# Optimization experiments

Measured on AMD Instinct MI355X. Metric: run time of the kernel, lower is better.

The kernel has to match this reference:

```python
import jax, jax.numpy as jnp
import numpy as np
from jax import lax

B, H, W = 4096, 8, 8
DICT, SE, E, NZ = 64, 8, 256, 1024
C1, C2 = 64, 128
EPS = 1e-4


def setup_inputs() -> dict:
    key = jax.random.key(0)
    ks = jax.random.split(key, 32)
    d = {}
    d['s'] = jax.random.randint(ks[0], (B, H, W), 0, DICT)
    d['s_prime'] = jax.random.randint(ks[1], (B, H, W), 0, DICT)
    d['w_embed'] = jax.random.normal(ks[2], (DICT, SE), dtype=jnp.float32)
    i = 3
    for p in ('p1', 'p2', 'p3'):
        d[p + '_w1'] = jax.random.normal(ks[i], (C1, SE, 3, 3), dtype=jnp.float32) * 0.1; i += 1
        d[p + '_b1'] = jax.random.normal(ks[i], (C1,), dtype=jnp.float32) * 0.1; i += 1
        d[p + '_w2'] = jax.random.normal(ks[i], (C2, C1, 3, 3), dtype=jnp.float32) * 0.05; i += 1
        d[p + '_b2'] = jax.random.normal(ks[i], (C2,), dtype=jnp.float32) * 0.05; i += 1
        d[p + '_lw'] = jax.random.normal(ks[i], (E, C2 * H * W), dtype=jnp.float32) * 0.02; i += 1
        d[p + '_lb'] = jax.random.normal(ks[i], (E,), dtype=jnp.float32) * 0.02; i += 1
    d['z_vectors'] = jax.random.normal(ks[i], (NZ, E), dtype=jnp.float32)
    d['scale'] = jnp.ones((1,), dtype=jnp.float32)
    return d


def _conv(x, w, b):
    # x: [B,C,H,W], w: [O,I,3,3], padding=1 == SAME for k=3
    y = lax.conv_general_dilated(x, w, (1, 1), 'SAME',
                                 dimension_numbers=('NCHW', 'OIHW', 'NCHW'))
    return y + b[None, :, None, None]


def _phi(x, w1, b1, w2, b2, lw, lb):
    # run_modules(..., last_activation=True): relu after every conv
    x = jax.nn.relu(_conv(x, w1, b1))
    x = jax.nn.relu(_conv(x, w2, b2))
    x = x.reshape(x.shape[0], -1)  # [B, C2*H*W]
    return x @ lw.T + lb  # [B, E]


def _normalized(m, eps):
    return m / (jnp.sqrt(jnp.sum(m * m, axis=1, keepdims=True)) + eps)


def reference(s, s_prime, w_embed,
              p1_w1, p1_b1, p1_w2, p1_b2, p1_lw, p1_lb,
              p2_w1, p2_b1, p2_w2, p2_b2, p2_lw, p2_lb,
              p3_w1, p3_b1, p3_w2, p3_b2, p3_lw, p3_lb,
              z_vectors, scale):
    # nn.Embedding(max_norm=1): renorm rows with norm > 1 to unit norm
    wn = jnp.sqrt(jnp.sum(w_embed * w_embed, axis=1, keepdims=True))
    w = w_embed * jnp.minimum(1.0, 1.0 / jnp.maximum(wn, 1e-7))
    s_embed = jnp.transpose(w[s], (0, 3, 1, 2))        # [B,SE,H,W]
    sp_embed = jnp.transpose(w[s_prime], (0, 3, 1, 2))  # embed_conv is None -> identity

    s_int = _phi(s_embed, p1_w1, p1_b1, p1_w2, p1_b2, p1_lw, p1_lb)            # phi1
    diff_int = _phi(sp_embed - s_embed, p2_w1, p2_b1, p2_w2, p2_b2, p2_lw, p2_lb)  # phi2
    sp_out = _normalized(_phi(sp_embed, p3_w1, p3_b1, p3_w2, p3_b2, p3_lw, p3_lb), EPS)  # phi3

    # quantize: cdist (p=2) against codebook, argmax (farthest, as in source), gather
    x2 = jnp.sum(diff_int * diff_int, axis=1, keepdims=True)      # [B,1]
    z2 = jnp.sum(z_vectors * z_vectors, axis=1)[None, :]          # [1,NZ]
    dist = jnp.sqrt(jnp.maximum(x2 + z2 - 2.0 * (diff_int @ z_vectors.T), 0.0))  # [B,NZ]
    z_inds = jnp.argmax(dist, axis=1)                              # [B]
    z_matrix = z_vectors[z_inds]                                   # [B,E]

    s_out = _normalized(s_int + z_matrix, EPS)                     # fc (fc_sizes=None)
    gram = s_out @ sp_out.T                                        # [B,B]
    return jnp.exp(scale) * gram
```

## Files before the change

### kernel.cpp

```cpp
#include <hip/hip_runtime.h>
#include <hip/hip_bf16.h>
#include <math.h>

#define NB 4096
#define SE 8
#define ND 64
#define C1 64
#define C2 128
#define NE 256
#define NZ 1024
#define CHUNK 2048
#define KACT 8192
#define KSPLIT 8

#define W1M_N (3*64*96)
#define W2M_N (3*128*576)
#define ZT_N  (256*1024)
#define PREP_TOTAL (W1M_N + W2M_N + ZT_N)
#define LW_N (NE*KACT)

typedef __attribute__((ext_vector_type(8))) short bf16x8;
typedef __attribute__((ext_vector_type(4))) float f32x4;
typedef __attribute__((ext_vector_type(8))) unsigned short u16x8;
typedef __attribute__((ext_vector_type(4))) unsigned short u16x4;

static __device__ __forceinline__ unsigned short f2bf(float v) {
  __hip_bfloat16 h = __float2bfloat16(v);
  return __builtin_bit_cast(unsigned short, h);
}
static __device__ __forceinline__ float bf2f(unsigned short u) {
  return __bfloat162float(__builtin_bit_cast(__hip_bfloat16, u));
}

__global__ __launch_bounds__(256) void prep_kernel(
    const float* __restrict__ w1_0, const float* __restrict__ w1_1, const float* __restrict__ w1_2,
    const float* __restrict__ w2_0, const float* __restrict__ w2_1, const float* __restrict__ w2_2,
    const float* __restrict__ z,
    unsigned short* __restrict__ w1mh, unsigned short* __restrict__ w1ml,
    unsigned short* __restrict__ w2mh, unsigned short* __restrict__ w2ml,
    float* __restrict__ zT)
{
  int idx = blockIdx.x * 256 + threadIdx.x;
  if (idx < W1M_N) {
    int p = idx / 6144; int r = idx - p*6144; int o = r / 96; int q = r - o*96;
    int j = q >> 3; int c = q & 7;
    const float* w1 = (p == 0) ? w1_0 : (p == 1) ? w1_1 : w1_2;
    float v = (j < 9) ? w1[o*72 + c*9 + j] : 0.f;
    unsigned short h = f2bf(v);
    w1mh[idx] = h;
    w1ml[idx] = f2bf(v - bf2f(h));
  } else if (idx < W1M_N + W2M_N) {
    int r0 = idx - W1M_N;
    int p = r0 / (128*576); int r = r0 - p*(128*576);
    int o = r / 576; int rem = r - o*576; int j = rem >> 6; int c = rem & 63;
    const float* w2 = (p == 0) ? w2_0 : (p == 1) ? w2_1 : w2_2;
    float v = w2[o*576 + c*9 + j];
    unsigned short h = f2bf(v);
    w2mh[r0] = h;
    w2ml[r0] = f2bf(v - bf2f(h));
  } else if (idx < PREP_TOTAL) {
    int r = idx - (W1M_N + W2M_N);
    int e = r >> 10, n = r & 1023;
    zT[r] = z[n*256 + e];
  }
}

__global__ __launch_bounds__(256) void prep_lw_kernel(
    const float* __restrict__ lw, unsigned short* __restrict__ lwh,
    unsigned short* __restrict__ lwl, int do_lo)
{
  int idx = blockIdx.x * 256 + threadIdx.x;
  float v = lw[idx];
  unsigned short h = f2bf(v);
  lwh[idx] = h;
  if (do_lo) lwl[idx] = f2bf(v - bf2f(h));
}

template<int PASSES>
__global__ __launch_bounds__(256, 2) void conv_phi_kernel(
    const int* __restrict__ s, const int* __restrict__ sp,
    const float* __restrict__ w_embed,
    const unsigned short* __restrict__ w1mh, const unsigned short* __restrict__ w1ml,
    const float* __restrict__ b1,
    const unsigned short* __restrict__ w2mh, const unsigned short* __restrict__ w2ml,
    const float* __restrict__ b2,
    unsigned short* __restrict__ acth, unsigned short* __restrict__ actl,
    int mode, int b_start)
{
  __shared__ float wtab[ND][SE];
  __shared__ int sidx[128];
  __shared__ int spidx[128];
  __shared__ __align__(16) unsigned short xph[2][960];
  __shared__ __align__(16) unsigned short xpl[2][960];
  __shared__ __align__(16) unsigned short c1h[2][7680];
  __shared__ __align__(16) unsigned short c1l[2][7680];

  const int tid = threadIdx.x;
  const int b0 = b_start + blockIdx.x * 2;

  {
    int4 z4 = {0,0,0,0};
    for (int t = tid; t < 240; t += 256) { ((int4*)xph)[t] = z4; ((int4*)xpl)[t] = z4; }
    for (int t = tid; t < 1920; t += 256) { ((int4*)c1h)[t] = z4; ((int4*)c1l)[t] = z4; }
  }

  if (tid < 128) sidx[tid] = s[b0*64 + tid];
  else spidx[tid - 128] = sp[b0*64 + tid - 128];
  if (tid < 64) {
    float v[SE]; float ss = 0.f;
    #pragma unroll
    for (int c = 0; c < SE; ++c) { v[c] = w_embed[tid*SE + c]; ss += v[c]*v[c]; }
    float nrm = sqrtf(ss);
    float sc = fminf(1.f, 1.f / fmaxf(nrm, 1e-7f));
    #pragma unroll
    for (int c = 0; c < SE; ++c) wtab[tid][c] = v[c] * sc;
  }
  __syncthreads();

  if (tid < 128) {
    const int im = tid >> 6;
    const int p = tid & 63;
    const int y = p >> 3, x = p & 7;
    const float* r0 = wtab[sidx[tid]];
    const float* r1 = wtab[spidx[tid]];
    u16x8 hv, lv;
    #pragma unroll
    for (int c = 0; c < SE; ++c) {
      float e0 = r0[c], e1 = r1[c];
      float v = (mode == 0) ? e0 : (mode == 1) ? (e1 - e0) : e1;
      unsigned short h = f2bf(v);
      hv[c] = h;
      lv[c] = f2bf(v - bf2f(h));
    }
    const int lin = (y + 1)*12 + (x + 1);
    *(u16x8*)(&xph[im][lin*8]) = hv;
    *(u16x8*)(&xpl[im][lin*8]) = lv;
  }
  __syncthreads();

  {
    const int lane = tid & 63, wid = tid >> 6;
    const int im = wid >> 1, ph = wid & 1;
    const int l15 = lane & 15, lk4 = lane >> 4;

    f32x4 a1[4][2];
    #pragma unroll
    for (int fm = 0; fm < 4; ++fm)
      #pragma unroll
      for (int nf = 0; nf < 2; ++nf) a1[fm][nf] = (f32x4){0.f,0.f,0.f,0.f};

    #pragma unroll
    for (int kk = 0; kk < 3; ++kk) {
      const int j = (kk << 2) + lk4;
      const int jc = (j > 8) ? 8 : j;
      const int dy = jc / 3, dx = jc - 3*(jc/3);
      bf16x8 Wh[4], Wl[4];
      #pragma unroll
      for (int fm = 0; fm < 4; ++fm) {
        const int o = (fm << 4) + l15;
        Wh[fm] = *(const bf16x8*)(w1mh + o*96 + (kk << 5) + (lk4 << 3));
        Wl[fm] = *(const bf16x8*)(w1ml + o*96 + (kk << 5) + (lk4 << 3));
      }
      #pragma unroll
      for (int nf = 0; nf < 2; ++nf) {
        const int p = (ph << 5) + (nf << 4) + l15;
        const int lin = ((p >> 3) + dy)*12 + (p & 7) + dx;
        const bf16x8 Xh = *(const bf16x8*)(&xph[im][lin << 3]);
        const bf16x8 Xl = *(const bf16x8*)(&xpl[im][lin << 3]);
        __builtin_amdgcn_s_setprio(1);
        #pragma unroll
        for (int fm = 0; fm < 4; ++fm) {
          a1[fm][nf] = __builtin_amdgcn_mfma_f32_16x16x32_bf16(Wh[fm], Xh, a1[fm][nf], 0, 0, 0);
          a1[fm][nf] = __builtin_amdgcn_mfma_f32_16x16x32_bf16(Wl[fm], Xh, a1[fm][nf], 0, 0, 0);
          a1[fm][nf] = __builtin_amdgcn_mfma_f32_16x16x32_bf16(Wh[fm], Xl, a1[fm][nf], 0, 0, 0);
        }
        __builtin_amdgcn_s_setprio(0);
      }
    }

    #pragma unroll
    for (int fm = 0; fm < 4; ++fm) {
      const int obase = (fm << 4) + (lk4 << 2);
      const float4 bv = *(const float4*)(b1 + obase);
      const int cb = obase >> 3;
      const int osub = obase & 7;
      #pragma unroll
      for (int nf = 0; nf < 2; ++nf) {
        const int p = (ph << 5) + (nf << 4) + l15;
        const int lin = ((p >> 3) + 1)*12 + (p & 7) + 1;
        const int idx2 = (lin << 6) + ((cb ^ (lin & 7)) << 3) + osub;
        u16x4 hv, lv;
        {
          float v0 = fmaxf(a1[fm][nf][0] + bv.x, 0.f);
          float v1 = fmaxf(a1[fm][nf][1] + bv.y, 0.f);
          float v2 = fmaxf(a1[fm][nf][2] + bv.z, 0.f);
          float v3 = fmaxf(a1[fm][nf][3] + bv.w, 0.f);
          hv[0] = f2bf(v0); hv[1] = f2bf(v1); hv[2] = f2bf(v2); hv[3] = f2bf(v3);
          lv[0] = f2bf(v0 - bf2f(hv[0])); lv[1] = f2bf(v1 - bf2f(hv[1]));
          lv[2] = f2bf(v2 - bf2f(hv[2])); lv[3] = f2bf(v3 - bf2f(hv[3]));
        }
        *(u16x4*)(&c1h[im][idx2]) = hv;
        *(u16x4*)(&c1l[im][idx2]) = lv;
      }
    }
  }
  __syncthreads();

  {
    const int lane = tid & 63, wid = tid >> 6;
    const int im = wid >> 1;
    const int ob = (wid & 1) << 6;
    const int l15 = lane & 15, lk4 = lane >> 4;
    const int y0b = l15 >> 3, x0 = l15 & 7;

    f32x4 acc[4][4];
    #pragma unroll
    for (int mf = 0; mf < 4; ++mf)
      #pragma unroll
      for (int nf = 0; nf < 4; ++nf) acc[mf][nf] = (f32x4){0.f,0.f,0.f,0.f};

    #pragma unroll
    for (int j = 0; j < 9; ++j) {
      const int dy = j / 3, dx = j - 3*(j/3);
      #pragma unroll
      for (int h2 = 0; h2 < 2; ++h2) {
        const int kofs = j*64 + h2*32 + lk4*8;
        bf16x8 Bh[4], Bl[4];
        #pragma unroll
        for (int nf = 0; nf < 4; ++nf) {
          const int orow = ob + (nf << 4) + l15;
          Bh[nf] = *(const bf16x8*)(w2mh + orow*576 + kofs);
          if (PASSES == 3) Bl[nf] = *(const bf16x8*)(w2ml + orow*576 + kofs);
        }
        const int cbk = (h2 << 2) + lk4;
        bf16x8 Ah[4], Al[4];
        #pragma unroll
        for (int mf = 0; mf < 4; ++mf) {
          const int lin = ((mf << 1) + y0b + dy)*12 + x0 + dx;
          const int idx2 = (lin << 6) + ((cbk ^ (lin & 7)) << 3);
          Ah[mf] = *(const bf16x8*)(&c1h[im][idx2]);
          Al[mf] = *(const bf16x8*)(&c1l[im][idx2]);
        }
        __builtin_amdgcn_s_setprio(1);
        #pragma unroll
        for (int mf = 0; mf < 4; ++mf) {
          #pragma unroll
          for (int nf = 0; nf < 4; ++nf) {
            acc[mf][nf] = __builtin_amdgcn_mfma_f32_16x16x32_bf16(Ah[mf], Bh[nf], acc[mf][nf], 0, 0, 0);
            acc[mf][nf] = __builtin_amdgcn_mfma_f32_16x16x32_bf16(Al[mf], Bh[nf], acc[mf][nf], 0, 0, 0);
            if (PASSES == 3)
              acc[mf][nf] = __builtin_amdgcn_mfma_f32_16x16x32_bf16(Ah[mf], Bl[nf], acc[mf][nf], 0, 0, 0);
          }
        }
        __builtin_amdgcn_s_setprio(0);
      }
    }

    const size_t rowbase = (size_t)(blockIdx.x*2 + im) * 8192;
    #pragma unroll
    for (int nf = 0; nf < 4; ++nf) {
      const int col = ob + (nf << 4) + l15;
      const float bv = b2[col];
      #pragma unroll
      for (int mf = 0; mf < 4; ++mf) {
        const int p0 = mf*16 + lk4*4;
        u16x4 hv, lv;
        #pragma unroll
        for (int r2 = 0; r2 < 4; ++r2) {
          float v = fmaxf(acc[mf][nf][r2] + bv, 0.f);
          unsigned short hq = f2bf(v);
          hv[r2] = hq;
          lv[r2] = f2bf(v - bf2f(hq));
        }
        *(u16x4*)(acth + rowbase + col*64 + p0) = hv;
        if (PASSES == 3)
          *(u16x4*)(actl + rowbase + col*64 + p0) = lv;
      }
    }
  }
}

template<int PASSES>
__global__ __launch_bounds__(256) void gemm_lds_tn(
    const unsigned short* __restrict__ Ahp, const unsigned short* __restrict__ Alp,
    const unsigned short* __restrict__ Bhp, const unsigned short* __restrict__ Blp,
    int K, float* __restrict__ Cdirect, float* __restrict__ Cpart,
    const float* __restrict__ bias, const float* __restrict__ scale_ptr)
{
  constexpr int NOP = (PASSES == 3) ? 2 : 1;
  __shared__ __align__(16) unsigned short As[NOP][128*64];
  __shared__ __align__(16) unsigned short Bs[NOP][64*64];

  const int tid = threadIdx.x;
  const int lane = tid & 63, wid = tid >> 6;
  const int wm = wid >> 1, wn = wid & 1;
  const int l15 = lane & 15, lk4 = lane >> 4;
  const int M = gridDim.x << 7, N = gridDim.y << 6;
  const int KC = K / gridDim.z;
  const int bm = blockIdx.x << 7, bn = blockIdx.y << 6;
  const int kbase = blockIdx.z * KC;
  const int NT = KC >> 6;

  const int sr = tid >> 3;
  const int sc8 = (tid & 7) * 8;

  const unsigned short* gA[NOP];
  const unsigned short* gB[NOP];
  gA[0] = Ahp; gB[0] = Bhp;
  if (PASSES == 3) { gA[1] = Alp; gB[1] = Blp; }

  u16x8 ra[NOP][4], rb[NOP][2];

  f32x4 acc[4][2];
  #pragma unroll
  for (int fm = 0; fm < 4; ++fm)
    #pragma unroll
    for (int nf = 0; nf < 2; ++nf) acc[fm][nf] = (f32x4){0.f,0.f,0.f,0.f};

  {
    const int k0 = kbase + sc8;
    #pragma unroll
    for (int p = 0; p < NOP; ++p) {
      #pragma unroll
      for (int i = 0; i < 4; ++i)
        ra[p][i] = *(const u16x8*)(gA[p] + (size_t)(bm + sr + i*32) * K + k0);
      #pragma unroll
      for (int i = 0; i < 2; ++i)
        rb[p][i] = *(const u16x8*)(gB[p] + (size_t)(bn + sr + i*32) * K + k0);
    }
  }

  for (int t = 0; t < NT; ++t) {
    __syncthreads();
    #pragma unroll
    for (int p = 0; p < NOP; ++p) {
      #pragma unroll
      for (int i = 0; i < 4; ++i) {
        const int r = sr + i*32;
        *(u16x8*)(&As[p][r*64 + (sc8 ^ ((r & 7) << 3))]) = ra[p][i];
      }
      #pragma unroll
      for (int i = 0; i < 2; ++i) {
        const int r = sr + i*32;
        *(u16x8*)(&Bs[p][r*64 + (sc8 ^ ((r & 7) << 3))]) = rb[p][i];
      }
    }
    __syncthreads();
    if (t + 1 < NT) {
      const int k0 = kbase + ((t + 1) << 6) + sc8;
      #pragma unroll
      for (int p = 0; p < NOP; ++p) {
        #pragma unroll
        for (int i = 0; i < 4; ++i)
          ra[p][i] = *(const u16x8*)(gA[p] + (size_t)(bm + sr + i*32) * K + k0);
        #pragma unroll
        for (int i = 0; i < 2; ++i)
          rb[p][i] = *(const u16x8*)(gB[p] + (size_t)(bn + sr + i*32) * K + k0);
      }
    }
    #pragma unroll
    for (int ks = 0; ks < 2; ++ks) {
      const int kb = ks*32 + lk4*8;
      bf16x8 af[NOP][4], bf[NOP][2];
      #pragma unroll
      for (int p = 0; p < NOP; ++p) {
        #pragma unroll
        for (int fm = 0; fm < 4; ++fm) {
          const int r = wm*64 + fm*16 + l15;
          af[p][fm] = *(const bf16x8*)(&As[p][r*64 + (kb ^ ((r & 7) << 3))]);
        }
        #pragma unroll
        for (int nf = 0; nf < 2; ++nf) {
          const int r = wn*32 + nf*16 + l15;
          bf[p][nf] = *(const bf16x8*)(&Bs[p][r*64 + (kb ^ ((r & 7) << 3))]);
        }
      }
      #pragma unroll
      for (int fm = 0; fm < 4; ++fm) {
        #pragma unroll
        for (int nf = 0; nf < 2; ++nf) {
          acc[fm][nf] = __builtin_amdgcn_mfma_f32_16x16x32_bf16(af[0][fm], bf[0][nf], acc[fm][nf], 0, 0, 0);
          if (PASSES == 3) {
            acc[fm][nf] = __builtin_amdgcn_mfma_f32_16x16x32_bf16(af[0][fm], bf[1][nf], acc[fm][nf], 0, 0, 0);
            acc[fm][nf] = __builtin_amdgcn_mfma_f32_16x16x32_bf16(af[1][fm], bf[0][nf], acc[fm][nf], 0, 0, 0);
          }
        }
      }
    }
  }

  if (Cpart) {
    float* base = Cpart + (size_t)blockIdx.z * ((size_t)M * N);
    #pragma unroll
    for (int fm = 0; fm < 4; ++fm) {
      #pragma unroll
      for (int nf = 0; nf < 2; ++nf) {
        const int row0 = bm + wm*64 + fm*16 + lk4*4;
        const int col  = bn + wn*32 + nf*16 + l15;
        #pragma unroll
        for (int r2 = 0; r2 < 4; ++r2)
          base[(size_t)(row0 + r2) * N + col] = acc[fm][nf][r2];
      }
    }
  } else {
    float alpha = scale_ptr ? expf(scale_ptr[0]) : 1.f;
    #pragma unroll
    for (int fm = 0; fm < 4; ++fm) {
      #pragma unroll
      for (int nf = 0; nf < 2; ++nf) {
        const int row0 = bm + wm*64 + fm*16 + lk4*4;
        const int col  = bn + wn*32 + nf*16 + l15;
        const float bv = bias ? bias[col] : 0.f;
        #pragma unroll
        for (int r2 = 0; r2 < 4; ++r2)
          Cdirect[(size_t)(row0 + r2) * N + col] = alpha * acc[fm][nf][r2] + bv;
      }
    }
  }
}

__global__ __launch_bounds__(256) void reduce_bias_kernel(
    const float* __restrict__ part, const float* __restrict__ bias, float* __restrict__ out)
{
  const int idx = blockIdx.x * 256 + threadIdx.x;
  float a = bias[idx & (NE-1)];
  #pragma unroll
  for (int q = 0; q < KSPLIT; ++q) a += part[(size_t)q * (CHUNK*NE) + idx];
  out[idx] = a;
}

__global__ __launch_bounds__(256) void quant_kernel(
    const float* __restrict__ diff, const float* __restrict__ zT, int* __restrict__ z_ind)
{
  __shared__ __align__(16) float d[8][NE];
  __shared__ float wv[8][4];
  __shared__ int wni[8][4];
  const int tid = threadIdx.x;
  const int b0 = blockIdx.x * 8;
  for (int j = tid; j < 8*NE; j += 256) (&d[0][0])[j] = diff[(size_t)b0*NE + j];
  __syncthreads();

  float zz[4] = {0.f, 0.f, 0.f, 0.f};
  float dot[8][4] = {};
  for (int e = 0; e < NE; e += 4) {
    float4 dd[8];
    #pragma unroll
    for (int r = 0; r < 8; ++r) dd[r] = *(const float4*)(&d[r][e]);
    #pragma unroll
    for (int u = 0; u < 4; ++u) {
      const float* zr = zT + (size_t)(e + u) * NZ + tid;
      float z0 = zr[0], z1 = zr[256], z2 = zr[512], z3 = zr[768];
      zz[0] = fmaf(z0, z0, zz[0]); zz[1] = fmaf(z1, z1, zz[1]);
      zz[2] = fmaf(z2, z2, zz[2]); zz[3] = fmaf(z3, z3, zz[3]);
      #pragma unroll
      for (int r = 0; r < 8; ++r) {
        const float de = (u == 0) ? dd[r].x : (u == 1) ? dd[r].y : (u == 2) ? dd[r].z : dd[r].w;
        dot[r][0] = fmaf(z0, de, dot[r][0]);
        dot[r][1] = fmaf(z1, de, dot[r][1]);
        dot[r][2] = fmaf(z2, de, dot[r][2]);
        dot[r][3] = fmaf(z3, de, dot[r][3]);
      }
    }
  }

  const int lane = tid & 63, wid = tid >> 6;
  #pragma unroll
  for (int r = 0; r < 8; ++r) {
    float best = zz[0] - 2.f*dot[r][0]; int bi = tid;
    float v1 = zz[1] - 2.f*dot[r][1]; if (v1 > best) { best = v1; bi = tid + 256; }
    float v2 = zz[2] - 2.f*dot[r][2]; if (v2 > best) { best = v2; bi = tid + 512; }
    float v3 = zz[3] - 2.f*dot[r][3]; if (v3 > best) { best = v3; bi = tid + 768; }
    for (int m = 1; m < 64; m <<= 1) {
      float ov = __shfl_xor(best, m, 64);
      int   oi = __shfl_xor(bi, m, 64);
      if (ov > best || (ov == best && oi < bi)) { best = ov; bi = oi; }
    }
    if (lane == 0) { wv[r][wid] = best; wni[r][wid] = bi; }
  }
  __syncthreads();
  if (tid < 8) {
    float best = wv[tid][0]; int bi = wni[tid][0];
    #pragma unroll
    for (int w = 1; w < 4; ++w) {
      float v = wv[tid][w]; int n = wni[tid][w];
      if (v > best || (v == best && n < bi)) { best = v; bi = n; }
    }
    z_ind[b0 + tid] = bi;
  }
}

__global__ __launch_bounds__(256) void norm_to_bf16_kernel(
    const float* __restrict__ v, unsigned short* __restrict__ ob)
{
  const int row = blockIdx.x*4 + (threadIdx.x >> 6);
  const int lane = threadIdx.x & 63;
  float4 x = ((const float4*)v)[(size_t)row*64 + lane];
  float ss = x.x*x.x + x.y*x.y + x.z*x.z + x.w*x.w;
  #pragma unroll
  for (int m = 1; m < 64; m <<= 1) ss += __shfl_xor(ss, m, 64);
  float sc = 1.f / (sqrtf(ss) + 1e-4f);
  u16x4 o;
  o[0] = f2bf(x.x*sc); o[1] = f2bf(x.y*sc); o[2] = f2bf(x.z*sc); o[3] = f2bf(x.w*sc);
  *(u16x4*)(ob + (size_t)row*NE + lane*4) = o;
}

__global__ __launch_bounds__(256) void build_sout_kernel(
    const float* __restrict__ s_int, const float* __restrict__ z,
    const int* __restrict__ z_ind, unsigned short* __restrict__ ob)
{
  const int row = blockIdx.x*4 + (threadIdx.x >> 6);
  const int lane = threadIdx.x & 63;
  const int zi = z_ind[row];
  float4 a = *((const float4*)s_int + (size_t)row*64 + lane);
  float4 c = *((const float4*)z + (size_t)zi*64 + lane);
  float4 x = {a.x + c.x, a.y + c.y, a.z + c.z, a.w + c.w};
  float ss = x.x*x.x + x.y*x.y + x.z*x.z + x.w*x.w;
  #pragma unroll
  for (int m = 1; m < 64; m <<= 1) ss += __shfl_xor(ss, m, 64);
  float sc = 1.f / (sqrtf(ss) + 1e-4f);
  u16x4 o;
  o[0] = f2bf(x.x*sc); o[1] = f2bf(x.y*sc); o[2] = f2bf(x.z*sc); o[3] = f2bf(x.w*sc);
  *(u16x4*)(ob + (size_t)row*NE + lane*4) = o;
}

extern "C" void kernel_launch(void* const* d_in, const int* in_sizes, int n_in,
                              void* d_out, int out_size, void* d_ws, size_t ws_size,
                              hipStream_t stream)
{
  const int* s  = (const int*)d_in[0];
  const int* sp = (const int*)d_in[1];
  const float* w_embed = (const float*)d_in[2];
  const float* z = (const float*)d_in[21];
  const float* scale = (const float*)d_in[22];
  float* out = (float*)d_out;

  size_t off = 0;
  auto allocB = [&](size_t bytes) -> void* {
    void* p = (void*)((char*)d_ws + off);
    off += ((bytes + 255) & ~(size_t)255);
    return p;
  };
  unsigned short* w1mh  = (unsigned short*)allocB((size_t)W1M_N * 2);
  unsigned short* w1ml  = (unsigned short*)allocB((size_t)W1M_N * 2);
  unsigned short* w2mh  = (unsigned short*)allocB((size_t)W2M_N * 2);
  unsigned short* w2ml  = (unsigned short*)allocB((size_t)W2M_N * 2);
  float* zT             = (float*)allocB(ZT_N * 4);
  unsigned short* lwh   = (unsigned short*)allocB((size_t)LW_N * 2);
  unsigned short* lwl   = (unsigned short*)allocB((size_t)LW_N * 2);
  float* s_int          = (float*)allocB((size_t)NB * NE * 4);
  float* diff_int       = (float*)allocB((size_t)NB * NE * 4);
  float* sp_out         = (float*)allocB((size_t)NB * NE * 4);
  unsigned short* soutb = (unsigned short*)allocB((size_t)NB * NE * 2);
  unsigned short* spoutb= (unsigned short*)allocB((size_t)NB * NE * 2);
  int*   z_ind          = (int*)allocB(NB * 4);
  float* part           = (float*)allocB((size_t)CHUNK * NE * KSPLIT * 4);

  unsigned short* acth = (unsigned short*)d_out;
  unsigned short* actl = acth + (size_t)CHUNK * KACT;

  prep_kernel<<<PREP_TOTAL/256, 256, 0, stream>>>(
      (const float*)d_in[3],  (const float*)d_in[9],  (const float*)d_in[15],
      (const float*)d_in[5],  (const float*)d_in[11], (const float*)d_in[17],
      z, w1mh, w1ml, w2mh, w2ml, zT);

  for (int phi = 0; phi < 3; ++phi) {
    const float* b1 = (const float*)d_in[4 + phi*6];
    const float* b2 = (const float*)d_in[6 + phi*6];
    const float* lw = (const float*)d_in[7 + phi*6];
    const float* lb = (const float*)d_in[8 + phi*6];
    float* outvec = (phi == 0) ? s_int : (phi == 1) ? diff_int : sp_out;

    prep_lw_kernel<<<LW_N/256, 256, 0, stream>>>(lw, lwh, lwl, phi == 1);

    for (int b0 = 0; b0 < NB; b0 += CHUNK) {
      if (phi == 1)
        conv_phi_kernel<3><<<CHUNK/2, 256, 0, stream>>>(
            s, sp, w_embed, w1mh + phi*6144, w1ml + phi*6144, b1,
            w2mh + phi*(128*576), w2ml + phi*(128*576), b2,
            acth, actl, phi, b0);
      else
        conv_phi_kernel<2><<<CHUNK/2, 256, 0, stream>>>(
            s, sp, w_embed, w1mh + phi*6144, w1ml + phi*6144, b1,
            w2mh + phi*(128*576), w2ml + phi*(128*576), b2,
            acth, actl, phi, b0);
      dim3 g(CHUNK/128, NE/64, KSPLIT);
      if (phi == 1)
        gemm_lds_tn<3><<<g, 256, 0, stream>>>(acth, actl, lwh, lwl,
            KACT, nullptr, part, nullptr, nullptr);
      else
        gemm_lds_tn<1><<<g, 256, 0, stream>>>(acth, nullptr, lwh, nullptr,
            KACT, nullptr, part, nullptr, nullptr);
      reduce_bias_kernel<<<(CHUNK*NE)/256, 256, 0, stream>>>(part, lb, outvec + (size_t)b0*NE);
    }
  }

  norm_to_bf16_kernel<<<NB/4, 256, 0, stream>>>(sp_out, spoutb);
  quant_kernel<<<NB/8, 256, 0, stream>>>(diff_int, zT, z_ind);
  build_sout_kernel<<<NB/4, 256, 0, stream>>>(s_int, z, z_ind, soutb);

  dim3 gg(NB/128, NB/64, 1);
  gemm_lds_tn<1><<<gg, 256, 0, stream>>>(soutb, nullptr, spoutb, nullptr,
      NE, out, nullptr, nullptr, scale);
}
```

Baseline: 641.8 us.

## Split fused conv kernel into separate conv1 and conv2 kernels via global scratch

The fused conv1+conv2 kernel is split into two kernels. convA computes conv1 for four images per block and writes the bf16 hi/lo activations to a global scratch buffer. convB reads those activations straight from global memory with bounds-checked padding and stages the conv2 weights through swizzled LDS, one 3x3 tap at a time. The aim is lower LDS use and higher occupancy, at the cost of an extra kernel launch and a global round trip for the conv1 activations.

```diff
diff --git a/kernel.cpp b/kernel.cpp
--- a/kernel.cpp
+++ b/kernel.cpp
@@ -76,36 +76,29 @@
   if (do_lo) lwl[idx] = f2bf(v - bf2f(h));
 }
 
-template<int PASSES>
-__global__ __launch_bounds__(256, 2) void conv_phi_kernel(
+__global__ __launch_bounds__(256, 3) void convA_kernel(
     const int* __restrict__ s, const int* __restrict__ sp,
     const float* __restrict__ w_embed,
     const unsigned short* __restrict__ w1mh, const unsigned short* __restrict__ w1ml,
     const float* __restrict__ b1,
-    const unsigned short* __restrict__ w2mh, const unsigned short* __restrict__ w2ml,
-    const float* __restrict__ b2,
-    unsigned short* __restrict__ acth, unsigned short* __restrict__ actl,
+    unsigned short* __restrict__ c1h, unsigned short* __restrict__ c1l,
     int mode, int b_start)
 {
   __shared__ float wtab[ND][SE];
-  __shared__ int sidx[128];
-  __shared__ int spidx[128];
-  __shared__ __align__(16) unsigned short xph[2][960];
-  __shared__ __align__(16) unsigned short xpl[2][960];
-  __shared__ __align__(16) unsigned short c1h[2][7680];
-  __shared__ __align__(16) unsigned short c1l[2][7680];
+  __shared__ __align__(16) unsigned short xph[4][960];
+  __shared__ __align__(16) unsigned short xpl[4][960];
 
   const int tid = threadIdx.x;
-  const int b0 = b_start + blockIdx.x * 2;
+  const int im = tid >> 6, p = tid & 63;
+  const int b = b_start + blockIdx.x*4 + im;
+
+  const int si  = s[b*64 + p];
+  const int spi = sp[b*64 + p];
 
   {
     int4 z4 = {0,0,0,0};
-    for (int t = tid; t < 240; t += 256) { ((int4*)xph)[t] = z4; ((int4*)xpl)[t] = z4; }
-    for (int t = tid; t < 1920; t += 256) { ((int4*)c1h)[t] = z4; ((int4*)c1l)[t] = z4; }
-  }
-
-  if (tid < 128) sidx[tid] = s[b0*64 + tid];
-  else spidx[tid - 128] = sp[b0*64 + tid - 128];
+    for (int t = tid; t < 480; t += 256) { ((int4*)xph)[t] = z4; ((int4*)xpl)[t] = z4; }
+  }
   if (tid < 64) {
     float v[SE]; float ss = 0.f;
     #pragma unroll
@@ -117,12 +110,9 @@
   }
   __syncthreads();
 
-  if (tid < 128) {
-    const int im = tid >> 6;
-    const int p = tid & 63;
-    const int y = p >> 3, x = p & 7;
-    const float* r0 = wtab[sidx[tid]];
-    const float* r1 = wtab[spidx[tid]];
+  {
+    const float* r0 = wtab[si];
+    const float* r1 = wtab[spi];
     u16x8 hv, lv;
     #pragma unroll
     for (int c = 0; c < SE; ++c) {
@@ -132,150 +122,181 @@
       hv[c] = h;
       lv[c] = f2bf(v - bf2f(h));
     }
-    const int lin = (y + 1)*12 + (x + 1);
+    const int lin = ((p >> 3) + 1)*12 + (p & 7) + 1;
     *(u16x8*)(&xph[im][lin*8]) = hv;
     *(u16x8*)(&xpl[im][lin*8]) = lv;
   }
   __syncthreads();
 
-  {
-    const int lane = tid & 63, wid = tid >> 6;
-    const int im = wid >> 1, ph = wid & 1;
-    const int l15 = lane & 15, lk4 = lane >> 4;
-
-    f32x4 a1[4][2];
-    #pragma unroll
-    for (int fm = 0; fm < 4; ++fm)
-      #pragma unroll
-      for (int nf = 0; nf < 2; ++nf) a1[fm][nf] = (f32x4){0.f,0.f,0.f,0.f};
-
-    #pragma unroll
-    for (int kk = 0; kk < 3; ++kk) {
-      const int j = (kk << 2) + lk4;
-      const int jc = (j > 8) ? 8 : j;
-      const int dy = jc / 3, dx = jc - 3*(jc/3);
-      bf16x8 Wh[4], Wl[4];
-      #pragma unroll
-      for (int fm = 0; fm < 4; ++fm) {
-        const int o = (fm << 4) + l15;
-        Wh[fm] = *(const bf16x8*)(w1mh + o*96 + (kk << 5) + (lk4 << 3));
-        Wl[fm] = *(const bf16x8*)(w1ml + o*96 + (kk << 5) + (lk4 << 3));
-      }
-      #pragma unroll
-      for (int nf = 0; nf < 2; ++nf) {
-        const int p = (ph << 5) + (nf << 4) + l15;
-        const int lin = ((p >> 3) + dy)*12 + (p & 7) + dx;
-        const bf16x8 Xh = *(const bf16x8*)(&xph[im][lin << 3]);
-        const bf16x8 Xl = *(const bf16x8*)(&xpl[im][lin << 3]);
-        __builtin_amdgcn_s_setprio(1);
-        #pragma unroll
-        for (int fm = 0; fm < 4; ++fm) {
-          a1[fm][nf] = __builtin_amdgcn_mfma_f32_16x16x32_bf16(Wh[fm], Xh, a1[fm][nf], 0, 0, 0);
-          a1[fm][nf] = __builtin_amdgcn_mfma_f32_16x16x32_bf16(Wl[fm], Xh, a1[fm][nf], 0, 0, 0);
-          a1[fm][nf] = __builtin_amdgcn_mfma_f32_16x16x32_bf16(Wh[fm], Xl, a1[fm][nf], 0, 0, 0);
+  const int lane = tid & 63, wid = tid >> 6;
+  const int l15 = lane & 15, lk4 = lane >> 4;
+
+  f32x4 a1[4][4];
+  #pragma unroll
+  for (int mf = 0; mf < 4; ++mf)
+    #pragma unroll
+    for (int nf = 0; nf < 4; ++nf) a1[mf][nf] = (f32x4){0.f,0.f,0.f,0.f};
+
+  #pragma unroll
+  for (int kk = 0; kk < 3; ++kk) {
+    const int j = (kk << 2) + lk4;
+    const int jc = (j > 8) ? 8 : j;
+    const int dy = jc / 3, dx = jc - 3*(jc/3);
+    bf16x8 Wh[4], Wl[4];
+    #pragma unroll
+    for (int mf = 0; mf < 4; ++mf) {
+      const int o = (mf << 4) + l15;
+      Wh[mf] = *(const bf16x8*)(w1mh + o*96 + (kk << 5) + (lk4 << 3));
+      Wl[mf] = *(const bf16x8*)(w1ml + o*96 + (kk << 5) + (lk4 << 3));
+    }
+    #pragma unroll
+    for (int nf = 0; nf < 4; ++nf) {
+      const int px = (nf << 4) + l15;
+      const int lin = ((px >> 3) + dy)*12 + (px & 7) + dx;
+      const bf16x8 Xh = *(const bf16x8*)(&xph[wid][lin << 3]);
+      const bf16x8 Xl = *(const bf16x8*)(&xpl[wid][lin << 3]);
+      __builtin_amdgcn_s_setprio(1);
+      #pragma unroll
+      for (int mf = 0; mf < 4; ++mf) {
+        a1[mf][nf] = __builtin_amdgcn_mfma_f32_16x16x32_bf16(Wh[mf], Xh, a1[mf][nf], 0, 0, 0);
+        a1[mf][nf] = __builtin_amdgcn_mfma_f32_16x16x32_bf16(Wl[mf], Xh, a1[mf][nf], 0, 0, 0);
+        a1[mf][nf] = __builtin_amdgcn_mfma_f32_16x16x32_bf16(Wh[mf], Xl, a1[mf][nf], 0, 0, 0);
+      }
+      __builtin_amdgcn_s_setprio(0);
+    }
+  }
+
+  const size_t cb = (size_t)(blockIdx.x*4 + wid) * 4096;
+  #pragma unroll
+  for (int mf = 0; mf < 4; ++mf) {
+    const int obase = (mf << 4) + (lk4 << 2);
+    const float4 bv = *(const float4*)(b1 + obase);
+    #pragma unroll
+    for (int nf = 0; nf < 4; ++nf) {
+      const int px = (nf << 4) + l15;
+      u16x4 hv, lv;
+      {
+        float v0 = fmaxf(a1[mf][nf][0] + bv.x, 0.f);
+        float v1 = fmaxf(a1[mf][nf][1] + bv.y, 0.f);
+        float v2 = fmaxf(a1[mf][nf][2] + bv.z, 0.f);
+        float v3 = fmaxf(a1[mf][nf][3] + bv.w, 0.f);
+        hv[0] = f2bf(v0); hv[1] = f2bf(v1); hv[2] = f2bf(v2); hv[3] = f2bf(v3);
+        lv[0] = f2bf(v0 - bf2f(hv[0])); lv[1] = f2bf(v1 - bf2f(hv[1]));
+        lv[2] = f2bf(v2 - bf2f(hv[2])); lv[3] = f2bf(v3 - bf2f(hv[3]));
+      }
+      *(u16x4*)(c1h + cb + px*64 + obase) = hv;
+      *(u16x4*)(c1l + cb + px*64 + obase) = lv;
+    }
+  }
+}
+
+template<int PASSES>
+__global__ __launch_bounds__(256, PASSES==3?2:3) void convB_kernel(
+    const unsigned short* __restrict__ c1h, const unsigned short* __restrict__ c1l,
+    const unsigned short* __restrict__ w2mh, const unsigned short* __restrict__ w2ml,
+    const float* __restrict__ b2,
+    unsigned short* __restrict__ acth, unsigned short* __restrict__ actl)
+{
+  __shared__ __align__(16) unsigned short Bsh[8192];
+  __shared__ __align__(16) unsigned short Bsl[PASSES==3 ? 8192 : 16];
+
+  const int tid = threadIdx.x;
+  const int lane = tid & 63, wid = tid >> 6;
+  const int img = blockIdx.x*2 + (wid >> 1);
+  const int ob = (wid & 1) << 6;
+  const int l15 = lane & 15, lk4 = lane >> 4;
+  const unsigned short* __restrict__ ch = c1h + (size_t)img*4096;
+  const unsigned short* __restrict__ cl = c1l + (size_t)img*4096;
+
+  const int so = tid >> 1;
+  const int sq = (tid & 1) << 5;
+
+  auto stage = [&](int j) {
+    const unsigned short* bh = w2mh + so*576 + j*64;
+    const unsigned short* bl = w2ml + so*576 + j*64;
+    #pragma unroll
+    for (int q = 0; q < 4; ++q) {
+      const int c = sq + q*8;
+      const int d = so*64 + (c ^ ((so & 7) << 3));
+      *(u16x8*)(&Bsh[d]) = *(const u16x8*)(bh + c);
+      if (PASSES == 3) *(u16x8*)(&Bsl[d]) = *(const u16x8*)(bl + c);
+    }
+  };
+
+  f32x4 acc[4][4];
+  #pragma unroll
+  for (int mf = 0; mf < 4; ++mf)
+    #pragma unroll
+    for (int nf = 0; nf < 4; ++nf) acc[mf][nf] = (f32x4){0.f,0.f,0.f,0.f};
+
+  stage(0);
+
+  for (int j = 0; j < 9; ++j) {
+    const int dy = j/3 - 1, dx = j - 3*(j/3) - 1;
+    bf16x8 Ah[2][4], Al[2][4];
+    #pragma unroll
+    for (int ks = 0; ks < 2; ++ks) {
+      #pragma unroll
+      for (int mf = 0; mf < 4; ++mf) {
+        const int px = (mf << 4) + l15;
+        const int yy = (px >> 3) + dy, xx = (px & 7) + dx;
+        bf16x8 vh = {0,0,0,0,0,0,0,0}, vl = {0,0,0,0,0,0,0,0};
+        if ((unsigned)yy < 8u && (unsigned)xx < 8u) {
+          const int a = ((yy << 3) + xx)*64 + (ks << 5) + (lk4 << 3);
+          vh = *(const bf16x8*)(ch + a);
+          vl = *(const bf16x8*)(cl + a);
         }
-        __builtin_amdgcn_s_setprio(0);
-      }
-    }
-
-    #pragma unroll
-    for (int fm = 0; fm < 4; ++fm) {
-      const int obase = (fm << 4) + (lk4 << 2);
-      const float4 bv = *(const float4*)(b1 + obase);
-      const int cb = obase >> 3;
-      const int osub = obase & 7;
-      #pragma unroll
-      for (int nf = 0; nf < 2; ++nf) {
-        const int p = (ph << 5) + (nf << 4) + l15;
-        const int lin = ((p >> 3) + 1)*12 + (p & 7) + 1;
-        const int idx2 = (lin << 6) + ((cb ^ (lin & 7)) << 3) + osub;
-        u16x4 hv, lv;
-        {
-          float v0 = fmaxf(a1[fm][nf][0] + bv.x, 0.f);
-          float v1 = fmaxf(a1[fm][nf][1] + bv.y, 0.f);
-          float v2 = fmaxf(a1[fm][nf][2] + bv.z, 0.f);
-          float v3 = fmaxf(a1[fm][nf][3] + bv.w, 0.f);
-          hv[0] = f2bf(v0); hv[1] = f2bf(v1); hv[2] = f2bf(v2); hv[3] = f2bf(v3);
-          lv[0] = f2bf(v0 - bf2f(hv[0])); lv[1] = f2bf(v1 - bf2f(hv[1]));
-          lv[2] = f2bf(v2 - bf2f(hv[2])); lv[3] = f2bf(v3 - bf2f(hv[3]));
+        Ah[ks][mf] = vh; Al[ks][mf] = vl;
+      }
+    }
+    __syncthreads();
+    #pragma unroll
+    for (int ks = 0; ks < 2; ++ks) {
+      const int kb = (ks << 5) + (lk4 << 3);
+      bf16x8 Bh[4], Bl[4];
+      #pragma unroll
+      for (int nf = 0; nf < 4; ++nf) {
+        const int r = ob + (nf << 4) + l15;
+        const int d = r*64 + (kb ^ ((r & 7) << 3));
+        Bh[nf] = *(const bf16x8*)(&Bsh[d]);
+        if (PASSES == 3) Bl[nf] = *(const bf16x8*)(&Bsl[d]);
+      }
+      __builtin_amdgcn_s_setprio(1);
+      #pragma unroll
+      for (int mf = 0; mf < 4; ++mf) {
+        #pragma unroll
+        for (int nf = 0; nf < 4; ++nf) {
+          acc[mf][nf] = __builtin_amdgcn_mfma_f32_16x16x32_bf16(Ah[ks][mf], Bh[nf], acc[mf][nf], 0, 0, 0);
+          acc[mf][nf] = __builtin_amdgcn_mfma_f32_16x16x32_bf16(Al[ks][mf], Bh[nf], acc[mf][nf], 0, 0, 0);
+          if (PASSES == 3)
+            acc[mf][nf] = __builtin_amdgcn_mfma_f32_16x16x32_bf16(Ah[ks][mf], Bl[nf], acc[mf][nf], 0, 0, 0);
         }
-        *(u16x4*)(&c1h[im][idx2]) = hv;
-        *(u16x4*)(&c1l[im][idx2]) = lv;
-      }
-    }
-  }
-  __syncthreads();
-
-  {
-    const int lane = tid & 63, wid = tid >> 6;
-    const int im = wid >> 1;
-    const int ob = (wid & 1) << 6;
-    const int l15 = lane & 15, lk4 = lane >> 4;
-    const int y0b = l15 >> 3, x0 = l15 & 7;
-
-    f32x4 acc[4][4];
-    #pragma unroll
-    for (int mf = 0; mf < 4; ++mf)
-      #pragma unroll
-      for (int nf = 0; nf < 4; ++nf) acc[mf][nf] = (f32x4){0.f,0.f,0.f,0.f};
-
-    #pragma unroll
-    for (int j = 0; j < 9; ++j) {
-      const int dy = j / 3, dx = j - 3*(j/3);
-      #pragma unroll
-      for (int h2 = 0; h2 < 2; ++h2) {
-        const int kofs = j*64 + h2*32 + lk4*8;
-        bf16x8 Bh[4], Bl[4];
-        #pragma unroll
-        for (int nf = 0; nf < 4; ++nf) {
-          const int orow = ob + (nf << 4) + l15;
-          Bh[nf] = *(const bf16x8*)(w2mh + orow*576 + kofs);
-          if (PASSES == 3) Bl[nf] = *(const bf16x8*)(w2ml + orow*576 + kofs);
-        }
-        const int cbk = (h2 << 2) + lk4;
-        bf16x8 Ah[4], Al[4];
-        #pragma unroll
-        for (int mf = 0; mf < 4; ++mf) {
-          const int lin = ((mf << 1) + y0b + dy)*12 + x0 + dx;
-          const int idx2 = (lin << 6) + ((cbk ^ (lin & 7)) << 3);
-          Ah[mf] = *(const bf16x8*)(&c1h[im][idx2]);
-          Al[mf] = *(const bf16x8*)(&c1l[im][idx2]);
-        }
-        __builtin_amdgcn_s_setprio(1);
-        #pragma unroll
-        for (int mf = 0; mf < 4; ++mf) {
-          #pragma unroll
-          for (int nf = 0; nf < 4; ++nf) {
-            acc[mf][nf] = __builtin_amdgcn_mfma_f32_16x16x32_bf16(Ah[mf], Bh[nf], acc[mf][nf], 0, 0, 0);
-            acc[mf][nf] = __builtin_amdgcn_mfma_f32_16x16x32_bf16(Al[mf], Bh[nf], acc[mf][nf], 0, 0, 0);
-            if (PASSES == 3)
-              acc[mf][nf] = __builtin_amdgcn_mfma_f32_16x16x32_bf16(Ah[mf], Bl[nf], acc[mf][nf], 0, 0, 0);
-          }
-        }
-        __builtin_amdgcn_s_setprio(0);
-      }
-    }
-
-    const size_t rowbase = (size_t)(blockIdx.x*2 + im) * 8192;
-    #pragma unroll
-    for (int nf = 0; nf < 4; ++nf) {
-      const int col = ob + (nf << 4) + l15;
-      const float bv = b2[col];
-      #pragma unroll
-      for (int mf = 0; mf < 4; ++mf) {
-        const int p0 = mf*16 + lk4*4;
-        u16x4 hv, lv;
-        #pragma unroll
-        for (int r2 = 0; r2 < 4; ++r2) {
-          float v = fmaxf(acc[mf][nf][r2] + bv, 0.f);
-          unsigned short hq = f2bf(v);
-          hv[r2] = hq;
-          lv[r2] = f2bf(v - bf2f(hq));
-        }
-        *(u16x4*)(acth + rowbase + col*64 + p0) = hv;
-        if (PASSES == 3)
-          *(u16x4*)(actl + rowbase + col*64 + p0) = lv;
-      }
+      }
+      __builtin_amdgcn_s_setprio(0);
+    }
+    __syncthreads();
+    if (j < 8) stage(j + 1);
+  }
+
+  const size_t rowbase = (size_t)img * 8192;
+  #pragma unroll
+  for (int nf = 0; nf < 4; ++nf) {
+    const int col = ob + (nf << 4) + l15;
+    const float bv = b2[col];
+    #pragma unroll
+    for (int mf = 0; mf < 4; ++mf) {
+      const int p0 = mf*16 + lk4*4;
+      u16x4 hv, lv;
+      #pragma unroll
+      for (int r2 = 0; r2 < 4; ++r2) {
+        float v = fmaxf(acc[mf][nf][r2] + bv, 0.f);
+        unsigned short hq = f2bf(v);
+        hv[r2] = hq;
+        lv[r2] = f2bf(v - bf2f(hq));
+      }
+      *(u16x4*)(acth + rowbase + col*64 + p0) = hv;
+      if (PASSES == 3)
+        *(u16x4*)(actl + rowbase + col*64 + p0) = lv;
     }
   }
 }
@@ -554,6 +575,8 @@
   unsigned short* spoutb= (unsigned short*)allocB((size_t)NB * NE * 2);
   int*   z_ind          = (int*)allocB(NB * 4);
   float* part           = (float*)allocB((size_t)CHUNK * NE * KSPLIT * 4);
+  unsigned short* c1h   = (unsigned short*)allocB((size_t)CHUNK * 4096 * 2);
+  unsigned short* c1l   = (unsigned short*)allocB((size_t)CHUNK * 4096 * 2);
 
   unsigned short* acth = (unsigned short*)d_out;
   unsigned short* actl = acth + (size_t)CHUNK * KACT;
@@ -573,16 +596,14 @@
     prep_lw_kernel<<<LW_N/256, 256, 0, stream>>>(lw, lwh, lwl, phi == 1);
 
     for (int b0 = 0; b0 < NB; b0 += CHUNK) {
+      convA_kernel<<<CHUNK/4, 256, 0, stream>>>(
+          s, sp, w_embed, w1mh + phi*6144, w1ml + phi*6144, b1, c1h, c1l, phi, b0);
       if (phi == 1)
-        conv_phi_kernel<3><<<CHUNK/2, 256, 0, stream>>>(
-            s, sp, w_embed, w1mh + phi*6144, w1ml + phi*6144, b1,
-            w2mh + phi*(128*576), w2ml + phi*(128*576), b2,
-            acth, actl, phi, b0);
+        convB_kernel<3><<<CHUNK/2, 256, 0, stream>>>(
+            c1h, c1l, w2mh + phi*(128*576), w2ml + phi*(128*576), b2, acth, actl);
       else
-        conv_phi_kernel<2><<<CHUNK/2, 256, 0, stream>>>(
-            s, sp, w_embed, w1mh + phi*6144, w1ml + phi*6144, b1,
-            w2mh + phi*(128*576), w2ml + phi*(128*576), b2,
-            acth, actl, phi, b0);
+        convB_kernel<2><<<CHUNK/2, 256, 0, stream>>>(
+            c1h, c1l, w2mh + phi*(128*576), w2ml + phi*(128*576), b2, acth, actl);
       dim3 g(CHUNK/128, NE/64, KSPLIT);
       if (phi == 1)
         gemm_lds_tn<3><<<g, 256, 0, stream>>>(acth, actl, lwh, lwl,
```

Result: slower. 966.0 us (+50.5%).
